# Optimization experiments

Hardware: AMD Instinct MI355X
Metric: run time of the kernel (lower is better)

## Reference

```python
import jax, jax.numpy as jnp
import numpy as np
from functools import partial

# Static configuration (must match setup_inputs / init_kwargs)
N_CLOUDS = 16      # number of point clouds in the batch
PTS = 16384        # points per cloud (uniform, batch vector is repeat(arange(B), PTS))
RATIO = 0.25       # EncodeLayer ratio
M = int(PTS * RATIO)  # samples per cloud = 4096


def _fps_one(p, m):
    """Farthest point sampling on one cloud p:[n,3] -> local indices [m].
    Matches torch_geometric fps with random_start=False semantics: start at point 0,
    then iteratively pick the point with max min-distance to the selected set."""
    d0 = jnp.sum((p - p[0]) ** 2, axis=-1)  # squared dist to first pick, [n]

    def step(dists, _):
        idx = jnp.argmax(dists)
        new_d = jnp.sum((p - p[idx]) ** 2, axis=-1)
        return jnp.minimum(dists, new_d), idx

    _, idxs = jax.lax.scan(step, d0, None, length=m - 1)
    return jnp.concatenate([jnp.zeros((1,), dtype=idxs.dtype), idxs])


def setup_inputs() -> dict:
    key = jax.random.key(0)
    k1, k2 = jax.random.split(key)
    pos = jax.random.normal(k1, (N_CLOUDS * PTS, 3), dtype=jnp.float32)
    feats = jax.random.normal(k2, (N_CLOUDS * PTS, 128), dtype=jnp.float32)
    batch = jnp.repeat(jnp.arange(N_CLOUDS, dtype=jnp.int64), PTS)
    return {"pos": pos, "feats": feats, "batch": batch}


def reference(pos, feats, batch):
    # pos:[N,3]; batch assumed uniform with N_CLOUDS clouds of PTS points each.
    pos_b = pos.reshape(N_CLOUDS, PTS, 3)
    local = jax.vmap(partial(_fps_one, m=M))(pos_b)  # [B, M] local indices
    offsets = (jnp.arange(N_CLOUDS, dtype=local.dtype) * PTS)[:, None]
    samples = (local + offsets).reshape(-1)  # global flat indices, like torch_geometric fps
    return samples
```

## Files before the change

### kernel.cpp

```cpp
#include <hip/hip_runtime.h>

#define N_CLOUDS 16
#define PTS      16384
#define M        4096
#define FPS_THREADS  1024
#define NWAVES   (FPS_THREADS / 64)
#define PPT      16
#define SORT_THREADS 512

typedef float v2f __attribute__((ext_vector_type(2)));
typedef unsigned long long u64;
typedef unsigned int u32;
typedef unsigned short u16;


#define PAIRS8_X(X) X(0) X(1) X(2) X(3) X(4) X(5) X(6) X(7)

#define DPP_MAX_STEP(key, CTRL) { \
        const u32 lo_  = (u32)(key); \
        const u32 hi_  = (u32)((key) >> 32); \
        const u32 lo2_ = (u32)__builtin_amdgcn_update_dpp(0, (int)lo_, (CTRL), 0xf, 0xf, false); \
        const u32 hi2_ = (u32)__builtin_amdgcn_update_dpp(0, (int)hi_, (CTRL), 0xf, 0xf, false); \
        const u64 ok_  = ((u64)hi2_ << 32) | lo2_; \
        (key) = (ok_ > (key)) ? ok_ : (key); \
    }

#define DPP_FMIN_STEP(v, CTRL) { \
        const int t_ = __builtin_amdgcn_update_dpp(__float_as_int(v), __float_as_int(v), (CTRL), 0xf, 0xf, false); \
        (v) = fminf((v), __int_as_float(t_)); \
    }
#define DPP_FMAX_STEP(v, CTRL) { \
        const int t_ = __builtin_amdgcn_update_dpp(__float_as_int(v), __float_as_int(v), (CTRL), 0xf, 0xf, false); \
        (v) = fmaxf((v), __int_as_float(t_)); \
    }
#define DPP_RED6(MACRO, v) \
        MACRO(v, 0x111) MACRO(v, 0x112) MACRO(v, 0x114) MACRO(v, 0x118) \
        MACRO(v, 0x142) MACRO(v, 0x143)
#define DPP_BFLY4(MACRO, v) \
        MACRO(v, 0xB1) MACRO(v, 0x4E) MACRO(v, 0x141) MACRO(v, 0x140)

#define BITONIC_PASS(KMAX) \
    for (u32 k = 2; k <= (u32)(KMAX); k <<= 1) { \
        for (u32 j = k >> 1; j; j >>= 1) { \
            __syncthreads(); \
            for (int s = 0; s < PTS / SORT_THREADS; ++s) { \
                const u32 i = (u32)(tid + s * SORT_THREADS); \
                const u32 p = i ^ j; \
                if (p > i) { \
                    const u32 a = keys[i], b = keys[p]; \
                    if (((i & k) == 0) == (a > b)) { keys[i] = b; keys[p] = a; } \
                } \
            } \
        } \
    } \
    __syncthreads();

__global__ __launch_bounds__(SORT_THREADS)
void sort_kernel(const float* __restrict__ pos, float* __restrict__ pos_s,
                 u16* __restrict__ mapT)
{
    __shared__ u32 keys[PTS];
    const int cloud = blockIdx.x;
    const int tid   = threadIdx.x;
    const int ln    = tid & 63;
    const size_t b3 = (size_t)cloud * PTS * 3;

    float mnx = 1e30f, mxx = -1e30f, mny = 1e30f, mxy = -1e30f;
    float mnz = 1e30f, mxz = -1e30f;
    for (int s = 0; s < PTS / SORT_THREADS; ++s) {
        const size_t o = b3 + (size_t)(tid + s * SORT_THREADS) * 3;
        const float x = pos[o + 0];
        const float y = pos[o + 1];
        const float z = pos[o + 2];
        mnx = fminf(mnx, x); mxx = fmaxf(mxx, x);
        mny = fminf(mny, y); mxy = fmaxf(mxy, y);
        mnz = fminf(mnz, z); mxz = fmaxf(mxz, z);
    }
    DPP_RED6(DPP_FMIN_STEP, mnx)
    DPP_RED6(DPP_FMAX_STEP, mxx)
    DPP_RED6(DPP_FMIN_STEP, mny)
    DPP_RED6(DPP_FMAX_STEP, mxy)
    DPP_RED6(DPP_FMIN_STEP, mnz)
    DPP_RED6(DPP_FMAX_STEP, mxz)
    float* red = (float*)keys;
    const int nw = SORT_THREADS / 64;
    if (ln == 63) {
        red[tid >> 6]          = mnx;
        red[nw + (tid >> 6)]   = mxx;
        red[2*nw + (tid >> 6)] = mny;
        red[3*nw + (tid >> 6)] = mxy;
        red[4*nw + (tid >> 6)] = mnz;
        red[5*nw + (tid >> 6)] = mxz;
    }
    __syncthreads();
    float xmin = red[0], xmax = red[nw], ymin = red[2*nw], ymax = red[3*nw];
    float zmin = red[4*nw], zmax = red[5*nw];
    for (int w = 1; w < nw; ++w) {
        xmin = fminf(xmin, red[w]);
        xmax = fmaxf(xmax, red[nw + w]);
        ymin = fminf(ymin, red[2*nw + w]);
        ymax = fmaxf(ymax, red[3*nw + w]);
        zmin = fminf(zmin, red[4*nw + w]);
        zmax = fmaxf(zmax, red[5*nw + w]);
    }
    __syncthreads();

    const float xscale = 262143.0f / fmaxf(xmax - xmin, 1e-30f);
    const float yscale = 262143.0f / fmaxf(ymax - ymin, 1e-30f);
    const float zscale = 262143.0f / fmaxf(zmax - zmin, 1e-30f);

    for (int s = 0; s < PTS / SORT_THREADS; ++s) {
        const int i = tid + s * SORT_THREADS;
        const float x = pos[b3 + (size_t)i * 3];
        const u32 q = (u32)fminf(fmaxf((x - xmin) * xscale, 0.0f), 262143.0f);
        keys[i] = (q << 14) | (u32)i;
    }
    BITONIC_PASS(PTS)

    for (int s = 0; s < PTS / SORT_THREADS; ++s) {
        const int i = tid + s * SORT_THREADS;
        const u32 orig = keys[i] & (u32)(PTS - 1);
        const float y = pos[b3 + (size_t)orig * 3 + 1];
        const u32 q = (u32)fminf(fmaxf((y - ymin) * yscale, 0.0f), 262143.0f);
        keys[i] = (q << 14) | orig;
    }
    BITONIC_PASS(4096u)

    for (int s = 0; s < PTS / SORT_THREADS; ++s) {
        const int i = tid + s * SORT_THREADS;
        const u32 orig = keys[i] & (u32)(PTS - 1);
        const float z = pos[b3 + (size_t)orig * 3 + 2];
        const u32 q = (u32)fminf(fmaxf((z - zmin) * zscale, 0.0f), 262143.0f);
        keys[i] = (q << 14) | orig;
    }
    BITONIC_PASS(1024u)

    for (int c = 0; c < 2; ++c) {
        u32 loc[PPT];
        const int cb = tid * 32 + c * PPT;
        for (int s = 0; s < PPT; ++s) loc[s] = keys[cb + s] & (u32)(PTS - 1);
        for (int a = 1; a < PPT; ++a) {
            const u32 v = loc[a];
            int b = a;
            while (b > 0 && loc[b - 1] > v) { loc[b] = loc[b - 1]; --b; }
            loc[b] = v;
        }
        for (int s = 0; s < PPT; ++s) keys[cb + s] = loc[s];
    }
    __syncthreads();

    for (int s = 0; s < PTS / SORT_THREADS; ++s) {
        const int i = tid + s * SORT_THREADS;
        const u32 orig = keys[i];
        mapT[(size_t)cloud * PTS + (size_t)(i & (PPT - 1)) * FPS_THREADS + (i >> 4)] = (u16)orig;
        const size_t so = b3 + (size_t)i * 3;
        const size_t oo = b3 + (size_t)orig * 3;
        pos_s[so + 0] = pos[oo + 0];
        pos_s[so + 1] = pos[oo + 1];
        pos_s[so + 2] = pos[oo + 2];
    }
}

#define WAVE_REDUCE(key, rkhi, rklo, chi, clo) { \
        DPP_MAX_STEP(key, 0xB1)   \
        DPP_MAX_STEP(key, 0x4E)   \
        DPP_MAX_STEP(key, 0x141)  \
        DPP_MAX_STEP(key, 0x140)  \
        rkhi = (u32)((key) >> 32); \
        rklo = (u32)(key); \
        DPP_MAX_STEP(key, 0x142)  \
        DPP_MAX_STEP(key, 0x143)  \
        chi = (u32)__builtin_amdgcn_readlane((int)(u32)((key) >> 32), 63); \
        clo = (u32)__builtin_amdgcn_readlane((int)(u32)(key), 63); \
    }

template<bool SORTED>
__global__ __launch_bounds__(FPS_THREADS)
__attribute__((amdgpu_waves_per_eu(4, 4)))
void fps_kernel(const float* __restrict__ pos,
                const float* __restrict__ psrc,
                const u16* __restrict__ mapT,
                int* __restrict__ out)
{
#pragma clang fp contract(off)
    const int cloud = blockIdx.x;
    const int tid   = threadIdx.x;
    const int base  = cloud * PTS;
    const int wave  = tid >> 6;
    const int lane  = tid & 63;

    __shared__ u64 skey[2][NWAVES];
    __shared__ __attribute__((aligned(16))) u16 mlds[PTS];

    if constexpr (SORTED) {
        const uint4* src = (const uint4*)(mapT + (size_t)cloud * PTS);
        uint4* dst = (uint4*)mlds;
#pragma unroll
        for (int s = 0; s < PTS * 2 / 16 / FPS_THREADS; ++s)
            dst[s * FPS_THREADS + tid] = src[s * FPS_THREADS + tid];
        __syncthreads();
    }

    const float q0x = pos[(size_t)base * 3 + 0];
    const float q0y = pos[(size_t)base * 3 + 1];
    const float q0z = pos[(size_t)base * 3 + 2];
    v2f qx2 = {q0x, q0x}, qy2 = {q0y, q0y}, qz2 = {q0z, q0z};

    const float4* pos4 = (const float4*)psrc;
    const int fo = cloud * (PTS * 3 / 4) + tid * (PPT * 3 / 4);

#define DECL(j) v2f XX##j, YY##j, ZZ##j, DD##j;
    PAIRS8_X(DECL)
#undef DECL

#define QUADLOAD(q, j0, j1) { \
        const float4 fa = pos4[fo + 3*(q) + 0]; \
        const float4 fb = pos4[fo + 3*(q) + 1]; \
        const float4 fc = pos4[fo + 3*(q) + 2]; \
        XX##j0 = (v2f){fa.x, fa.w}; \
        YY##j0 = (v2f){fa.y, fb.x}; \
        ZZ##j0 = (v2f){fa.z, fb.y}; \
        XX##j1 = (v2f){fb.z, fc.y}; \
        YY##j1 = (v2f){fb.w, fc.z}; \
        ZZ##j1 = (v2f){fc.x, fc.w}; }
    QUADLOAD(0, 0, 1) QUADLOAD(1, 2, 3) QUADLOAD(2, 4, 5) QUADLOAD(3, 6, 7)
#undef QUADLOAD

#define PIN8(a,b,c,d,e,g,h,k) asm volatile("" : "+v"(a),"+v"(b),"+v"(c),"+v"(d),"+v"(e),"+v"(g),"+v"(h),"+v"(k));
    PIN8(XX0, XX1, XX2, XX3, XX4, XX5, XX6, XX7)
    PIN8(YY0, YY1, YY2, YY3, YY4, YY5, YY6, YY7)
    PIN8(ZZ0, ZZ1, ZZ2, ZZ3, ZZ4, ZZ5, ZZ6, ZZ7)
#undef PIN8

    float rxlo, rxhi, rylo, ryhi, rzlo, rzhi;
    {
        float mnx = fminf(XX0.x, XX0.y), mxx = fmaxf(XX0.x, XX0.y);
        float mny = fminf(YY0.x, YY0.y), mxy = fmaxf(YY0.x, YY0.y);
        float mnz = fminf(ZZ0.x, ZZ0.y), mxz = fmaxf(ZZ0.x, ZZ0.y);
#define MINMAX(j) { mnx = fminf(mnx, fminf(XX##j.x, XX##j.y)); \
                    mxx = fmaxf(mxx, fmaxf(XX##j.x, XX##j.y)); \
                    mny = fminf(mny, fminf(YY##j.x, YY##j.y)); \
                    mxy = fmaxf(mxy, fmaxf(YY##j.x, YY##j.y)); \
                    mnz = fminf(mnz, fminf(ZZ##j.x, ZZ##j.y)); \
                    mxz = fmaxf(mxz, fmaxf(ZZ##j.x, ZZ##j.y)); }
        MINMAX(1) MINMAX(2) MINMAX(3) MINMAX(4) MINMAX(5) MINMAX(6) MINMAX(7)
#undef MINMAX
        DPP_BFLY4(DPP_FMIN_STEP, mnx)
        DPP_BFLY4(DPP_FMAX_STEP, mxx)
        DPP_BFLY4(DPP_FMIN_STEP, mny)
        DPP_BFLY4(DPP_FMAX_STEP, mxy)
        DPP_BFLY4(DPP_FMIN_STEP, mnz)
        DPP_BFLY4(DPP_FMAX_STEP, mxz)
        rxlo = mnx; rxhi = mxx; rylo = mny; ryhi = mxy; rzlo = mnz; rzhi = mxz;
    }

    float bd = -1.0f;
    int   bk = 0;
#define INITP(j) { \
        v2f dx = XX##j - qx2; \
        v2f dy = YY##j - qy2; \
        v2f dz = ZZ##j - qz2; \
        v2f nd = (dx * dx + dy * dy) + dz * dz; \
        DD##j = nd; \
        if (nd.x > bd) { bd = nd.x; bk = 2*(j); } \
        if (nd.y > bd) { bd = nd.y; bk = 2*(j) + 1; } \
    }
    PAIRS8_X(INITP)
#undef INITP

    if (tid == 0) out[cloud * M] = base;

    u32 rk_hi, rk_lo, c_hi, c_lo;
    {
        int bi;
        if constexpr (SORTED) bi = (int)mlds[(bk << 10) + tid];
        else                  bi = tid * PPT + bk;
        u64 key = ((u64)__float_as_uint(bd) << 32) | (u32)(~bi);
        WAVE_REDUCE(key, rk_hi, rk_lo, c_hi, c_lo)
    }

    for (int i = 1; i < M; ++i) {
        if (lane == 0) skey[i & 1][wave] = ((u64)c_hi << 32) | c_lo;
        __syncthreads();

        u64 key2 = skey[i & 1][lane & 15];
        DPP_MAX_STEP(key2, 0x111)
        DPP_MAX_STEP(key2, 0x112)
        DPP_MAX_STEP(key2, 0x114)
        DPP_MAX_STEP(key2, 0x118)
        const u32 wlo = (u32)__builtin_amdgcn_readlane((int)(u32)key2, 15);
        const int wi  = (int)(~wlo);

        if (tid == 0) out[cloud * M + i] = base + wi;

        const float* qp = pos + (size_t)(base + wi) * 3;
        const float qx = qp[0], qy = qp[1], qz = qp[2];

        const float dxg = fmaxf(fmaxf(rxlo - qx, qx - rxhi), 0.0f);
        const float dyg = fmaxf(fmaxf(rylo - qy, qy - ryhi), 0.0f);
        const float dzg = fmaxf(fmaxf(rzlo - qz, qz - rzhi), 0.0f);
        const float lb  = (dxg * dxg + dyg * dyg + dzg * dzg) * 0.9999f;
        if (!__all(lb > __uint_as_float(rk_hi))) {
            qx2 = (v2f){qx, qx}; qy2 = (v2f){qy, qy}; qz2 = (v2f){qz, qz};
            bd = -1.0f; bk = 0;
#define UPD(j) { \
        v2f dx = XX##j - qx2; \
        v2f dy = YY##j - qy2; \
        v2f dz = ZZ##j - qz2; \
        v2f nd = (dx * dx + dy * dy) + dz * dz; \
        DD##j.x = fminf(DD##j.x, nd.x); \
        DD##j.y = fminf(DD##j.y, nd.y); \
        if (DD##j.x > bd) { bd = DD##j.x; bk = 2*(j); } \
        if (DD##j.y > bd) { bd = DD##j.y; bk = 2*(j) + 1; } \
    }
            PAIRS8_X(UPD)
#undef UPD
            int bi;
            if constexpr (SORTED) bi = (int)mlds[(bk << 10) + tid];
            else                  bi = tid * PPT + bk;
            u64 key = ((u64)__float_as_uint(bd) << 32) | (u32)(~bi);
            WAVE_REDUCE(key, rk_hi, rk_lo, c_hi, c_lo)
        }
    }
}

extern "C" void kernel_launch(void* const* d_in, const int* in_sizes, int n_in,
                              void* d_out, int out_size, void* d_ws, size_t ws_size,
                              hipStream_t stream) {
    const float* pos = (const float*)d_in[0];
    int* out = (int*)d_out;

    const size_t pos_s_bytes = (size_t)N_CLOUDS * PTS * 3 * sizeof(float);
    const size_t map_bytes   = (size_t)N_CLOUDS * PTS * sizeof(u16);
    if (d_ws && ws_size >= pos_s_bytes + map_bytes) {
        float* pos_s = (float*)d_ws;
        u16*   mapT  = (u16*)((char*)d_ws + pos_s_bytes);
        sort_kernel<<<N_CLOUDS, SORT_THREADS, 0, stream>>>(pos, pos_s, mapT);
        fps_kernel<true><<<N_CLOUDS, FPS_THREADS, 0, stream>>>(pos, pos_s, mapT, out);
    } else {
        fps_kernel<false><<<N_CLOUDS, FPS_THREADS, 0, stream>>>(pos, pos, nullptr, out);
    }
}
```

Baseline: 4.400 ms.

## Commit two FPS picks per iteration using top-2 reduction with validity check

Each thread now keeps its top-2 candidate distances, and the block reduces both the best and the runner-up key. When the runner-up is provably still the next farthest point after updating with the first pick (its distance to the first pick is at least its current min-distance, and no point ties it), both are committed in one iteration. This can roughly halve the number of block-wide barrier rounds. The cost is extra reductions, a second barrier plus a shared flag in dual iterations, and more register pressure. The box culling test becomes per-thread rather than per-wave, and the sort kernel moves to 1024 threads with one 16-element chunk each.

```diff
diff --git a/kernel.cpp b/kernel.cpp
--- a/kernel.cpp
+++ b/kernel.cpp
@@ -6,7 +6,7 @@
 #define FPS_THREADS  1024
 #define NWAVES   (FPS_THREADS / 64)
 #define PPT      16
-#define SORT_THREADS 512
+#define SORT_THREADS 1024
 
 typedef float v2f __attribute__((ext_vector_type(2)));
 typedef unsigned long long u64;
@@ -36,8 +36,15 @@
 #define DPP_RED6(MACRO, v) \
         MACRO(v, 0x111) MACRO(v, 0x112) MACRO(v, 0x114) MACRO(v, 0x118) \
         MACRO(v, 0x142) MACRO(v, 0x143)
-#define DPP_BFLY4(MACRO, v) \
-        MACRO(v, 0xB1) MACRO(v, 0x4E) MACRO(v, 0x141) MACRO(v, 0x140)
+
+#define CHAIN6_MAX(key) \
+        DPP_MAX_STEP(key, 0x111) DPP_MAX_STEP(key, 0x112) \
+        DPP_MAX_STEP(key, 0x114) DPP_MAX_STEP(key, 0x118) \
+        DPP_MAX_STEP(key, 0x142) DPP_MAX_STEP(key, 0x143)
+
+#define BFLY4_MAX(key) \
+        DPP_MAX_STEP(key, 0xB1) DPP_MAX_STEP(key, 0x4E) \
+        DPP_MAX_STEP(key, 0x141) DPP_MAX_STEP(key, 0x140)
 
 #define BITONIC_PASS(KMAX) \
     for (u32 k = 2; k <= (u32)(KMAX); k <<= 1) { \
@@ -135,9 +142,9 @@
     }
     BITONIC_PASS(1024u)
 
-    for (int c = 0; c < 2; ++c) {
+    {
         u32 loc[PPT];
-        const int cb = tid * 32 + c * PPT;
+        const int cb = tid * PPT;
         for (int s = 0; s < PPT; ++s) loc[s] = keys[cb + s] & (u32)(PTS - 1);
         for (int a = 1; a < PPT; ++a) {
             const u32 v = loc[a];
@@ -160,19 +167,6 @@
         pos_s[so + 2] = pos[oo + 2];
     }
 }
-
-#define WAVE_REDUCE(key, rkhi, rklo, chi, clo) { \
-        DPP_MAX_STEP(key, 0xB1)   \
-        DPP_MAX_STEP(key, 0x4E)   \
-        DPP_MAX_STEP(key, 0x141)  \
-        DPP_MAX_STEP(key, 0x140)  \
-        rkhi = (u32)((key) >> 32); \
-        rklo = (u32)(key); \
-        DPP_MAX_STEP(key, 0x142)  \
-        DPP_MAX_STEP(key, 0x143)  \
-        chi = (u32)__builtin_amdgcn_readlane((int)(u32)((key) >> 32), 63); \
-        clo = (u32)__builtin_amdgcn_readlane((int)(u32)(key), 63); \
-    }
 
 template<bool SORTED>
 __global__ __launch_bounds__(FPS_THREADS)
@@ -189,22 +183,24 @@
     const int wave  = tid >> 6;
     const int lane  = tid & 63;
 
-    __shared__ u64 skey[2][NWAVES];
+    __shared__ u64 skA[2][NWAVES];
+    __shared__ u64 skB[2][NWAVES];
+    __shared__ u32 vflag[2];
     __shared__ __attribute__((aligned(16))) u16 mlds[PTS];
 
+    if (tid == 0) { vflag[0] = 0; vflag[1] = 0; }
     if constexpr (SORTED) {
         const uint4* src = (const uint4*)(mapT + (size_t)cloud * PTS);
         uint4* dst = (uint4*)mlds;
 #pragma unroll
         for (int s = 0; s < PTS * 2 / 16 / FPS_THREADS; ++s)
             dst[s * FPS_THREADS + tid] = src[s * FPS_THREADS + tid];
-        __syncthreads();
-    }
+    }
+    __syncthreads();
 
     const float q0x = pos[(size_t)base * 3 + 0];
     const float q0y = pos[(size_t)base * 3 + 1];
     const float q0z = pos[(size_t)base * 3 + 2];
-    v2f qx2 = {q0x, q0x}, qy2 = {q0y, q0y}, qz2 = {q0z, q0z};
 
     const float4* pos4 = (const float4*)psrc;
     const int fo = cloud * (PTS * 3 / 4) + tid * (PPT * 3 / 4);
@@ -232,7 +228,7 @@
     PIN8(ZZ0, ZZ1, ZZ2, ZZ3, ZZ4, ZZ5, ZZ6, ZZ7)
 #undef PIN8
 
-    float rxlo, rxhi, rylo, ryhi, rzlo, rzhi;
+    float cxlo, cxhi, cylo, cyhi, czlo, czhi;
     {
         float mnx = fminf(XX0.x, XX0.y), mxx = fmaxf(XX0.x, XX0.y);
         float mny = fminf(YY0.x, YY0.y), mxy = fmaxf(YY0.x, YY0.y);
@@ -245,82 +241,153 @@
                     mxz = fmaxf(mxz, fmaxf(ZZ##j.x, ZZ##j.y)); }
         MINMAX(1) MINMAX(2) MINMAX(3) MINMAX(4) MINMAX(5) MINMAX(6) MINMAX(7)
 #undef MINMAX
-        DPP_BFLY4(DPP_FMIN_STEP, mnx)
-        DPP_BFLY4(DPP_FMAX_STEP, mxx)
-        DPP_BFLY4(DPP_FMIN_STEP, mny)
-        DPP_BFLY4(DPP_FMAX_STEP, mxy)
-        DPP_BFLY4(DPP_FMIN_STEP, mnz)
-        DPP_BFLY4(DPP_FMAX_STEP, mxz)
-        rxlo = mnx; rxhi = mxx; rylo = mny; ryhi = mxy; rzlo = mnz; rzhi = mxz;
-    }
-
-    float bd = -1.0f;
-    int   bk = 0;
+        cxlo = mnx; cxhi = mxx; cylo = mny; cyhi = mxy; czlo = mnz; czhi = mxz;
+    }
+
+    {
+        const v2f qx2 = {q0x, q0x}, qy2 = {q0y, q0y}, qz2 = {q0z, q0z};
 #define INITP(j) { \
         v2f dx = XX##j - qx2; \
         v2f dy = YY##j - qy2; \
         v2f dz = ZZ##j - qz2; \
-        v2f nd = (dx * dx + dy * dy) + dz * dz; \
-        DD##j = nd; \
-        if (nd.x > bd) { bd = nd.x; bk = 2*(j); } \
-        if (nd.y > bd) { bd = nd.y; bk = 2*(j) + 1; } \
-    }
-    PAIRS8_X(INITP)
+        DD##j = (dx * dx + dy * dy) + dz * dz; }
+        PAIRS8_X(INITP)
 #undef INITP
+    }
 
     if (tid == 0) out[cloud * M] = base;
 
-    u32 rk_hi, rk_lo, c_hi, c_lo;
-    {
-        int bi;
-        if constexpr (SORTED) bi = (int)mlds[(bk << 10) + tid];
-        else                  bi = tid * PPT + bk;
-        u64 key = ((u64)__float_as_uint(bd) << 32) | (u32)(~bi);
-        WAVE_REDUCE(key, rk_hi, rk_lo, c_hi, c_lo)
-    }
-
-    for (int i = 1; i < M; ++i) {
-        if (lane == 0) skey[i & 1][wave] = ((u64)c_hi << 32) | c_lo;
+    float bd, bd2; int bk, bk2;
+    u32 c_hi, c_lo, k2_hi, k2_lo;
+#define TOP2H(v, s) { \
+        const bool c1 = (v) > bd; \
+        const bool c2 = (v) > bd2; \
+        const float nb2 = c1 ? bd : (c2 ? (v) : bd2); \
+        const int   nk2 = c1 ? bk : (c2 ? (s) : bk2); \
+        bd  = c1 ? (v) : bd;  bk  = c1 ? (s) : bk; \
+        bd2 = nb2;            bk2 = nk2; }
+#define TOP2P(j) TOP2H(DD##j.x, 2*(j)) TOP2H(DD##j.y, 2*(j)+1)
+#define FINALIZE() { \
+        bd = -1.0f; bk = 0; bd2 = -1.0f; bk2 = 0; \
+        PAIRS8_X(TOP2P) \
+        int bi_, bi2_; \
+        if constexpr (SORTED) { bi_  = (int)mlds[(bk  << 10) + tid]; \
+                                bi2_ = (int)mlds[(bk2 << 10) + tid]; } \
+        else                  { bi_  = tid * PPT + bk; \
+                                bi2_ = tid * PPT + bk2; } \
+        const u64 key1  = ((u64)__float_as_uint(bd)  << 32) | (u32)(~bi_); \
+        const u64 key2v = ((u64)__float_as_uint(bd2) << 32) | (u32)(~bi2_); \
+        u64 t_ = key1; \
+        CHAIN6_MAX(t_) \
+        c_hi = (u32)__builtin_amdgcn_readlane((int)(u32)(t_ >> 32), 63); \
+        c_lo = (u32)__builtin_amdgcn_readlane((int)(u32)t_, 63); \
+        const u64 cc_ = ((u64)c_hi << 32) | c_lo; \
+        u64 sub_ = (key1 == cc_) ? key2v : key1; \
+        CHAIN6_MAX(sub_) \
+        k2_hi = (u32)__builtin_amdgcn_readlane((int)(u32)(sub_ >> 32), 63); \
+        k2_lo = (u32)__builtin_amdgcn_readlane((int)(u32)sub_, 63); }
+
+    FINALIZE()
+
+    int i = 1, par = 0;
+    while (i < M) {
+        if (lane == 0) {
+            skA[par][wave] = ((u64)c_hi << 32) | c_lo;
+            skB[par][wave] = ((u64)k2_hi << 32) | k2_lo;
+        }
+        if (tid == 0) vflag[par ^ 1] = 0;
         __syncthreads();
 
-        u64 key2 = skey[i & 1][lane & 15];
-        DPP_MAX_STEP(key2, 0x111)
-        DPP_MAX_STEP(key2, 0x112)
-        DPP_MAX_STEP(key2, 0x114)
-        DPP_MAX_STEP(key2, 0x118)
-        const u32 wlo = (u32)__builtin_amdgcn_readlane((int)(u32)key2, 15);
-        const int wi  = (int)(~wlo);
-
-        if (tid == 0) out[cloud * M + i] = base + wi;
-
-        const float* qp = pos + (size_t)(base + wi) * 3;
-        const float qx = qp[0], qy = qp[1], qz = qp[2];
-
-        const float dxg = fmaxf(fmaxf(rxlo - qx, qx - rxhi), 0.0f);
-        const float dyg = fmaxf(fmaxf(rylo - qy, qy - ryhi), 0.0f);
-        const float dzg = fmaxf(fmaxf(rzlo - qz, qz - rzhi), 0.0f);
-        const float lb  = (dxg * dxg + dyg * dyg + dzg * dzg) * 0.9999f;
-        if (!__all(lb > __uint_as_float(rk_hi))) {
-            qx2 = (v2f){qx, qx}; qy2 = (v2f){qy, qy}; qz2 = (v2f){qz, qz};
-            bd = -1.0f; bk = 0;
-#define UPD(j) { \
-        v2f dx = XX##j - qx2; \
-        v2f dy = YY##j - qy2; \
-        v2f dz = ZZ##j - qz2; \
-        v2f nd = (dx * dx + dy * dy) + dz * dz; \
-        DD##j.x = fminf(DD##j.x, nd.x); \
-        DD##j.y = fminf(DD##j.y, nd.y); \
-        if (DD##j.x > bd) { bd = DD##j.x; bk = 2*(j); } \
-        if (DD##j.y > bd) { bd = DD##j.y; bk = 2*(j) + 1; } \
-    }
-            PAIRS8_X(UPD)
-#undef UPD
-            int bi;
-            if constexpr (SORTED) bi = (int)mlds[(bk << 10) + tid];
-            else                  bi = tid * PPT + bk;
-            u64 key = ((u64)__float_as_uint(bd) << 32) | (u32)(~bi);
-            WAVE_REDUCE(key, rk_hi, rk_lo, c_hi, c_lo)
+        const u64 a = skA[par][lane & 15];
+        const u64 b = skB[par][lane & 15];
+        u64 g1 = a;
+        BFLY4_MAX(g1)
+        const bool isw = (a == g1);
+        u64 r_ = isw ? 0ull : a;
+        BFLY4_MAX(r_)
+        const unsigned long long ball = __ballot(isw && (lane < 16));
+        const int ws = (int)__ffsll(ball) - 1;
+        const u32 bwlo = (u32)__builtin_amdgcn_readlane((int)(u32)b, ws);
+        const u32 bwhi = (u32)__builtin_amdgcn_readlane((int)(u32)(b >> 32), ws);
+        const u64 k2w = ((u64)bwhi << 32) | bwlo;
+        const u64 g2 = (k2w > r_) ? k2w : r_;
+
+        const u32 g1lo_s = (u32)__builtin_amdgcn_readfirstlane((int)(u32)g1);
+        const u32 g2lo_s = (u32)__builtin_amdgcn_readfirstlane((int)(u32)g2);
+        const u32 g2hi_s = (u32)__builtin_amdgcn_readfirstlane((int)(u32)(g2 >> 32));
+        const int wi1 = (int)(~g1lo_s);
+        const int wi2 = (int)(~g2lo_s);
+        if (tid == 0) out[cloud * M + i] = base + wi1;
+
+        const float* p1 = pos + (size_t)(base + wi1) * 3;
+        const float qx = p1[0], qy = p1[1], qz = p1[2];
+        const float* p2 = pos + (size_t)(base + wi2) * 3;
+        const float bx = p2[0], by = p2[1], bz = p2[2];
+
+        const float ddb2 = __uint_as_float(g2hi_s);
+        const float tdx = bx - qx, tdy = by - qy, tdz = bz - qz;
+        const float d2q = (tdx * tdx + tdy * tdy) + tdz * tdz;
+        const bool dual = (d2q >= ddb2) && (i + 1 < M);
+
+        const float q2x = dual ? bx : qx;
+        const float q2y = dual ? by : qy;
+        const float q2z = dual ? bz : qz;
+
+        const float ax = fmaxf(fmaxf(cxlo - qx, qx - cxhi), 0.0f);
+        const float ay = fmaxf(fmaxf(cylo - qy, qy - cyhi), 0.0f);
+        const float az = fmaxf(fmaxf(czlo - qz, qz - czhi), 0.0f);
+        const float lb1 = (ax * ax + ay * ay) + az * az;
+        const float ex = fmaxf(fmaxf(cxlo - q2x, q2x - cxhi), 0.0f);
+        const float ey = fmaxf(fmaxf(cylo - q2y, q2y - cyhi), 0.0f);
+        const float ez = fmaxf(fmaxf(czlo - q2z, q2z - czhi), 0.0f);
+        const float lb2 = (ex * ex + ey * ey) + ez * ez;
+        const bool skip = (lb1 * 0.9999f > bd) && (lb2 * 0.9999f > bd);
+        const bool act = !__all(skip);
+
+        int viol = 0;
+        if (act) {
+            const v2f qxa = {qx, qx}, qya = {qy, qy}, qza = {qz, qz};
+#define UPD1V(j) { \
+        v2f dx = XX##j - qxa; v2f dy = YY##j - qya; v2f dz = ZZ##j - qza; \
+        v2f n1 = (dx * dx + dy * dy) + dz * dz; \
+        viol |= ((n1.x == ddb2) && (DD##j.x > ddb2)) ? 1 : 0; \
+        viol |= ((n1.y == ddb2) && (DD##j.y > ddb2)) ? 1 : 0; \
+        DD##j.x = fminf(DD##j.x, n1.x); \
+        DD##j.y = fminf(DD##j.y, n1.y); }
+#define UPD1P(j) { \
+        v2f dx = XX##j - qxa; v2f dy = YY##j - qya; v2f dz = ZZ##j - qza; \
+        v2f n1 = (dx * dx + dy * dy) + dz * dz; \
+        DD##j.x = fminf(DD##j.x, n1.x); \
+        DD##j.y = fminf(DD##j.y, n1.y); }
+            if (dual) { PAIRS8_X(UPD1V) } else { PAIRS8_X(UPD1P) }
+#undef UPD1V
+#undef UPD1P
         }
+
+        bool commit2 = false;
+        if (dual) {
+            if (act && __any(viol) && lane == 0) vflag[par] = 1;
+            __syncthreads();
+            commit2 = (vflag[par] == 0);
+            if (commit2) {
+                if (tid == 0) out[cloud * M + i + 1] = base + wi2;
+                if (act) {
+                    const v2f qxb = {q2x, q2x}, qyb = {q2y, q2y}, qzb = {q2z, q2z};
+#define UPD2(j) { \
+        v2f dx = XX##j - qxb; v2f dy = YY##j - qyb; v2f dz = ZZ##j - qzb; \
+        v2f n2 = (dx * dx + dy * dy) + dz * dz; \
+        DD##j.x = fminf(DD##j.x, n2.x); \
+        DD##j.y = fminf(DD##j.y, n2.y); }
+                    PAIRS8_X(UPD2)
+#undef UPD2
+                }
+            }
+        }
+
+        if (act) FINALIZE()
+
+        par ^= 1;
+        i += commit2 ? 2 : 1;
     }
 }
 
```

Measured after the change: 8.018 ms. 82.2% more time.

## Broadcast winner coordinates via LDS and use fast 32-bit max reduction

Applied to the files above, without the earlier changes.

The FPS loop now has the owning lane write the winning point's coordinates into LDS next to the per-wave key. This removes the dependent global load of the selected point from the serial critical path. Wave and block reductions first do a 32-bit max on distance and fall back to a 64-bit key reduction only on ties. The culling bound is switched from a per-4-lane-group bbox to a per-thread bbox compared against the thread's own best distance, and the sort kernel moves to 1024 threads. The tie handling and bound change add branching and carry a small risk to tie semantics.

```diff
diff --git a/kernel.cpp b/kernel.cpp
--- a/kernel.cpp
+++ b/kernel.cpp
@@ -6,7 +6,7 @@
 #define FPS_THREADS  1024
 #define NWAVES   (FPS_THREADS / 64)
 #define PPT      16
-#define SORT_THREADS 512
+#define SORT_THREADS 1024
 
 typedef float v2f __attribute__((ext_vector_type(2)));
 typedef unsigned long long u64;
@@ -25,6 +25,11 @@
         (key) = (ok_ > (key)) ? ok_ : (key); \
     }
 
+#define DPP_MAXU_STEP(v, CTRL) { \
+        const u32 t_ = (u32)__builtin_amdgcn_update_dpp(0, (int)(v), (CTRL), 0xf, 0xf, false); \
+        (v) = (t_ > (v)) ? t_ : (v); \
+    }
+
 #define DPP_FMIN_STEP(v, CTRL) { \
         const int t_ = __builtin_amdgcn_update_dpp(__float_as_int(v), __float_as_int(v), (CTRL), 0xf, 0xf, false); \
         (v) = fminf((v), __int_as_float(t_)); \
@@ -36,8 +41,22 @@
 #define DPP_RED6(MACRO, v) \
         MACRO(v, 0x111) MACRO(v, 0x112) MACRO(v, 0x114) MACRO(v, 0x118) \
         MACRO(v, 0x142) MACRO(v, 0x143)
-#define DPP_BFLY4(MACRO, v) \
-        MACRO(v, 0xB1) MACRO(v, 0x4E) MACRO(v, 0x141) MACRO(v, 0x140)
+
+#define CHAIN6_MAX(key) \
+        DPP_MAX_STEP(key, 0x111) DPP_MAX_STEP(key, 0x112) \
+        DPP_MAX_STEP(key, 0x114) DPP_MAX_STEP(key, 0x118) \
+        DPP_MAX_STEP(key, 0x142) DPP_MAX_STEP(key, 0x143)
+#define CHAIN6_MAXU(v) \
+        DPP_MAXU_STEP(v, 0x111) DPP_MAXU_STEP(v, 0x112) \
+        DPP_MAXU_STEP(v, 0x114) DPP_MAXU_STEP(v, 0x118) \
+        DPP_MAXU_STEP(v, 0x142) DPP_MAXU_STEP(v, 0x143)
+
+#define BFLY4_MAX(key) \
+        DPP_MAX_STEP(key, 0xB1) DPP_MAX_STEP(key, 0x4E) \
+        DPP_MAX_STEP(key, 0x141) DPP_MAX_STEP(key, 0x140)
+#define BFLY4_MAXU(v) \
+        DPP_MAXU_STEP(v, 0xB1) DPP_MAXU_STEP(v, 0x4E) \
+        DPP_MAXU_STEP(v, 0x141) DPP_MAXU_STEP(v, 0x140)
 
 #define BITONIC_PASS(KMAX) \
     for (u32 k = 2; k <= (u32)(KMAX); k <<= 1) { \
@@ -135,9 +154,9 @@
     }
     BITONIC_PASS(1024u)
 
-    for (int c = 0; c < 2; ++c) {
+    {
         u32 loc[PPT];
-        const int cb = tid * 32 + c * PPT;
+        const int cb = tid * PPT;
         for (int s = 0; s < PPT; ++s) loc[s] = keys[cb + s] & (u32)(PTS - 1);
         for (int a = 1; a < PPT; ++a) {
             const u32 v = loc[a];
@@ -160,19 +179,6 @@
         pos_s[so + 2] = pos[oo + 2];
     }
 }
-
-#define WAVE_REDUCE(key, rkhi, rklo, chi, clo) { \
-        DPP_MAX_STEP(key, 0xB1)   \
-        DPP_MAX_STEP(key, 0x4E)   \
-        DPP_MAX_STEP(key, 0x141)  \
-        DPP_MAX_STEP(key, 0x140)  \
-        rkhi = (u32)((key) >> 32); \
-        rklo = (u32)(key); \
-        DPP_MAX_STEP(key, 0x142)  \
-        DPP_MAX_STEP(key, 0x143)  \
-        chi = (u32)__builtin_amdgcn_readlane((int)(u32)((key) >> 32), 63); \
-        clo = (u32)__builtin_amdgcn_readlane((int)(u32)(key), 63); \
-    }
 
 template<bool SORTED>
 __global__ __launch_bounds__(FPS_THREADS)
@@ -190,6 +196,7 @@
     const int lane  = tid & 63;
 
     __shared__ u64 skey[2][NWAVES];
+    __shared__ float scx[2][NWAVES], scy[2][NWAVES], scz[2][NWAVES];
     __shared__ __attribute__((aligned(16))) u16 mlds[PTS];
 
     if constexpr (SORTED) {
@@ -204,7 +211,6 @@
     const float q0x = pos[(size_t)base * 3 + 0];
     const float q0y = pos[(size_t)base * 3 + 1];
     const float q0z = pos[(size_t)base * 3 + 2];
-    v2f qx2 = {q0x, q0x}, qy2 = {q0y, q0y}, qz2 = {q0z, q0z};
 
     const float4* pos4 = (const float4*)psrc;
     const int fo = cloud * (PTS * 3 / 4) + tid * (PPT * 3 / 4);
@@ -232,7 +238,7 @@
     PIN8(ZZ0, ZZ1, ZZ2, ZZ3, ZZ4, ZZ5, ZZ6, ZZ7)
 #undef PIN8
 
-    float rxlo, rxhi, rylo, ryhi, rzlo, rzhi;
+    float cxlo, cxhi, cylo, cyhi, czlo, czhi;
     {
         float mnx = fminf(XX0.x, XX0.y), mxx = fmaxf(XX0.x, XX0.y);
         float mny = fminf(YY0.x, YY0.y), mxy = fmaxf(YY0.x, YY0.y);
@@ -245,17 +251,13 @@
                     mxz = fmaxf(mxz, fmaxf(ZZ##j.x, ZZ##j.y)); }
         MINMAX(1) MINMAX(2) MINMAX(3) MINMAX(4) MINMAX(5) MINMAX(6) MINMAX(7)
 #undef MINMAX
-        DPP_BFLY4(DPP_FMIN_STEP, mnx)
-        DPP_BFLY4(DPP_FMAX_STEP, mxx)
-        DPP_BFLY4(DPP_FMIN_STEP, mny)
-        DPP_BFLY4(DPP_FMAX_STEP, mxy)
-        DPP_BFLY4(DPP_FMIN_STEP, mnz)
-        DPP_BFLY4(DPP_FMAX_STEP, mxz)
-        rxlo = mnx; rxhi = mxx; rylo = mny; ryhi = mxy; rzlo = mnz; rzhi = mxz;
+        cxlo = mnx; cxhi = mxx; cylo = mny; cyhi = mxy; czlo = mnz; czhi = mxz;
     }
 
     float bd = -1.0f;
     int   bk = 0;
+    {
+        const v2f qx2 = {q0x, q0x}, qy2 = {q0y, q0y}, qz2 = {q0z, q0z};
 #define INITP(j) { \
         v2f dx = XX##j - qx2; \
         v2f dy = YY##j - qy2; \
@@ -265,43 +267,87 @@
         if (nd.x > bd) { bd = nd.x; bk = 2*(j); } \
         if (nd.y > bd) { bd = nd.y; bk = 2*(j) + 1; } \
     }
-    PAIRS8_X(INITP)
+        PAIRS8_X(INITP)
 #undef INITP
+    }
 
     if (tid == 0) out[cloud * M] = base;
 
-    u32 rk_hi, rk_lo, c_hi, c_lo;
-    {
-        int bi;
-        if constexpr (SORTED) bi = (int)mlds[(bk << 10) + tid];
-        else                  bi = tid * PPT + bk;
-        u64 key = ((u64)__float_as_uint(bd) << 32) | (u32)(~bi);
-        WAVE_REDUCE(key, rk_hi, rk_lo, c_hi, c_lo)
-    }
-
+    u32 c_hi, c_lo;
+    bool isown;
+    float qpx = 0.0f, qpy = 0.0f, qpz = 0.0f;
+#define FINALIZE() { \
+        int bi_; \
+        if constexpr (SORTED) bi_ = (int)mlds[(bk << 10) + tid]; \
+        else                  bi_ = tid * PPT + bk; \
+        const u32 nbi_ = ~(u32)bi_; \
+        const u32 db_  = __float_as_uint(bd); \
+        u32 mx_ = db_; \
+        CHAIN6_MAXU(mx_) \
+        const u32 wmax_ = (u32)__builtin_amdgcn_readlane((int)mx_, 63); \
+        const unsigned long long bl_ = __ballot(db_ == wmax_); \
+        if (__popcll(bl_) == 1) { \
+            const int ow_ = (int)__ffsll(bl_) - 1; \
+            c_hi = wmax_; \
+            c_lo = (u32)__builtin_amdgcn_readlane((int)nbi_, ow_); \
+            isown = (lane == ow_); \
+        } else { \
+            u64 key_ = ((u64)db_ << 32) | nbi_; \
+            CHAIN6_MAX(key_) \
+            c_hi = (u32)__builtin_amdgcn_readlane((int)(u32)(key_ >> 32), 63); \
+            c_lo = (u32)__builtin_amdgcn_readlane((int)(u32)key_, 63); \
+            isown = (db_ == c_hi) && (nbi_ == c_lo); \
+        } \
+        if (isown) { \
+            const float* pp_ = pos + (size_t)(base + bi_) * 3; \
+            qpx = pp_[0]; qpy = pp_[1]; qpz = pp_[2]; \
+        } \
+    }
+
+    FINALIZE()
+
+    int par = 0;
     for (int i = 1; i < M; ++i) {
-        if (lane == 0) skey[i & 1][wave] = ((u64)c_hi << 32) | c_lo;
+        if (lane == 0) skey[par][wave] = ((u64)c_hi << 32) | c_lo;
+        if (isown) {
+            scx[par][wave] = qpx;
+            scy[par][wave] = qpy;
+            scz[par][wave] = qpz;
+        }
         __syncthreads();
 
-        u64 key2 = skey[i & 1][lane & 15];
-        DPP_MAX_STEP(key2, 0x111)
-        DPP_MAX_STEP(key2, 0x112)
-        DPP_MAX_STEP(key2, 0x114)
-        DPP_MAX_STEP(key2, 0x118)
-        const u32 wlo = (u32)__builtin_amdgcn_readlane((int)(u32)key2, 15);
-        const int wi  = (int)(~wlo);
-
-        if (tid == 0) out[cloud * M + i] = base + wi;
-
-        const float* qp = pos + (size_t)(base + wi) * 3;
-        const float qx = qp[0], qy = qp[1], qz = qp[2];
-
-        const float dxg = fmaxf(fmaxf(rxlo - qx, qx - rxhi), 0.0f);
-        const float dyg = fmaxf(fmaxf(rylo - qy, qy - ryhi), 0.0f);
-        const float dzg = fmaxf(fmaxf(rzlo - qz, qz - rzhi), 0.0f);
-        const float lb  = (dxg * dxg + dyg * dyg + dzg * dzg) * 0.9999f;
-        if (!__all(lb > __uint_as_float(rk_hi))) {
-            qx2 = (v2f){qx, qx}; qy2 = (v2f){qy, qy}; qz2 = (v2f){qz, qz};
+        const u64 a  = skey[par][lane & 15];
+        const float kx = scx[par][lane & 15];
+        const float ky = scy[par][lane & 15];
+        const float kz = scz[par][lane & 15];
+
+        const u32 ahi = (u32)(a >> 32);
+        u32 mh = ahi;
+        BFLY4_MAXU(mh)
+        const unsigned long long ball = __ballot(ahi == mh) & 0xFFFFull;
+        int ws; u32 wlo;
+        if (__popcll(ball) == 1) {
+            ws  = (int)__ffsll(ball) - 1;
+            wlo = (u32)__builtin_amdgcn_readlane((int)(u32)a, ws);
+        } else {
+            u64 g = a;
+            BFLY4_MAX(g)
+            const unsigned long long b2 = __ballot(a == g) & 0xFFFFull;
+            ws  = (int)__ffsll(b2) - 1;
+            wlo = (u32)__builtin_amdgcn_readfirstlane((int)(u32)g);
+        }
+        if (tid == 0) out[cloud * M + i] = base + (int)(~wlo);
+
+        const float qx = __int_as_float(__builtin_amdgcn_readlane(__float_as_int(kx), ws));
+        const float qy = __int_as_float(__builtin_amdgcn_readlane(__float_as_int(ky), ws));
+        const float qz = __int_as_float(__builtin_amdgcn_readlane(__float_as_int(kz), ws));
+
+        const float ax = fmaxf(fmaxf(cxlo - qx, qx - cxhi), 0.0f);
+        const float ay = fmaxf(fmaxf(cylo - qy, qy - cyhi), 0.0f);
+        const float az = fmaxf(fmaxf(czlo - qz, qz - czhi), 0.0f);
+        const float lb = (ax * ax + ay * ay) + az * az;
+        if (!__all(lb * 0.9999f > bd)) {
+            const v2f qx2 = {qx, qx}, qy2 = {qy, qy}, qz2 = {qz, qz};
             bd = -1.0f; bk = 0;
 #define UPD(j) { \
         v2f dx = XX##j - qx2; \
@@ -315,12 +361,10 @@
     }
             PAIRS8_X(UPD)
 #undef UPD
-            int bi;
-            if constexpr (SORTED) bi = (int)mlds[(bk << 10) + tid];
-            else                  bi = tid * PPT + bk;
-            u64 key = ((u64)__float_as_uint(bd) << 32) | (u32)(~bi);
-            WAVE_REDUCE(key, rk_hi, rk_lo, c_hi, c_lo)
+            FINALIZE()
         }
+
+        par ^= 1;
     }
 }
 
```

Result: faster. 4.313 ms (-2.0%).
